# Performance work log

Hardware: AMD Instinct MI355X
Metric: run time of the kernel (lower is better)

The kernel has to match this reference:

```python
import jax, jax.numpy as jnp
import numpy as np

D_MODEL = 1024
NUM_HEADS = 16
D_K = D_MODEL // NUM_HEADS


def setup_inputs() -> dict:
    key = jax.random.key(0)
    ks = jax.random.split(key, 9)
    s = 1.0 / np.sqrt(D_MODEL)
    inp = {
        "x": jax.random.normal(ks[0], (2, 2048, D_MODEL), dtype=jnp.float32),
        "Wq": jax.random.uniform(ks[1], (D_MODEL, D_MODEL), jnp.float32, -s, s),
        "bq": jax.random.uniform(ks[2], (D_MODEL,), jnp.float32, -s, s),
        "Wk": jax.random.uniform(ks[3], (D_MODEL, D_MODEL), jnp.float32, -s, s),
        "bk": jax.random.uniform(ks[4], (D_MODEL,), jnp.float32, -s, s),
        "Wv": jax.random.uniform(ks[5], (D_MODEL, D_MODEL), jnp.float32, -s, s),
        "bv": jax.random.uniform(ks[6], (D_MODEL,), jnp.float32, -s, s),
        "Wo": jax.random.uniform(ks[7], (D_MODEL, D_MODEL), jnp.float32, -s, s),
        "bo": jax.random.uniform(ks[8], (D_MODEL,), jnp.float32, -s, s),
    }
    return inp


def reference(x, Wq, bq, Wk, bk, Wv, bv, Wo, bo):
    B, S, _ = x.shape
    # projections (torch Linear: y = x @ W.T + b)
    q = x @ Wq.T + bq
    k = x @ Wk.T + bk
    v = x @ Wv.T + bv
    # [B, H, S, Dk]
    q = q.reshape(B, S, NUM_HEADS, D_K).transpose(0, 2, 1, 3)
    k = k.reshape(B, S, NUM_HEADS, D_K).transpose(0, 2, 1, 3)
    v = v.reshape(B, S, NUM_HEADS, D_K).transpose(0, 2, 1, 3)
    scale = 1.0 / np.sqrt(D_K).astype(np.float32)
    energy = jnp.einsum("bhqd,bhkd->bhqk", q, k) * scale
    attn = jax.nn.softmax(energy, axis=-1)
    out = jnp.einsum("bhqk,bhkd->bhqd", attn, v)
    out = out.transpose(0, 2, 1, 3).reshape(B, S, D_MODEL)
    return out @ Wo.T + bo
```

## Files before the change

### kernel.cpp

```cpp
#include <hip/hip_runtime.h>
#include <hip/hip_bf16.h>
#include <cstdint>

typedef __bf16 bf16;
typedef __bf16 bf16x4 __attribute__((ext_vector_type(4)));
typedef __bf16 bf16x8 __attribute__((ext_vector_type(8)));
typedef float f32x4 __attribute__((ext_vector_type(4)));
typedef float f32x16 __attribute__((ext_vector_type(16)));
typedef unsigned int u32x4 __attribute__((ext_vector_type(4)));

#define DM   1024
#define SEQ  2048
#define NH   16
#define DKH  64

__device__ __forceinline__ bf16x8 ld8(const bf16* p) {
    return *reinterpret_cast<const bf16x8*>(p);
}

__device__ __forceinline__ void gld16(const void* g, void* lds) {
    __builtin_amdgcn_global_load_lds(
        (__attribute__((address_space(1))) void*)(uintptr_t)g,
        (__attribute__((address_space(3))) void*)(uint32_t)(uintptr_t)lds,
        16, 0, 0);
}

__device__ __forceinline__ f32x4 mfma16(bf16x8 a, bf16x8 b, f32x4 c) {
    return __builtin_amdgcn_mfma_f32_16x16x32_bf16(a, b, c, 0, 0, 0);
}
__device__ __forceinline__ f32x16 mfma32(bf16x8 a, bf16x8 b, f32x16 c) {
    return __builtin_amdgcn_mfma_f32_32x32x16_bf16(a, b, c, 0, 0, 0);
}

__device__ __forceinline__ unsigned pkbf(float lo, float hi) {
    unsigned r;
    asm("v_cvt_pk_bf16_f32 %0, %1, %2" : "=v"(r) : "v"(lo), "v"(hi));
    return r;
}
__device__ __forceinline__ void plswap(unsigned& a, unsigned& b) {
    asm volatile("v_permlane32_swap_b32 %0, %1" : "+v"(a), "+v"(b));
}

__global__ __launch_bounds__(256) void cvt_all(
    const float4* __restrict__ x,  const float4* __restrict__ wq,
    const float4* __restrict__ wk, const float4* __restrict__ wv,
    const float4* __restrict__ wo,
    ushort4* __restrict__ xb,  ushort4* __restrict__ wqb,
    ushort4* __restrict__ wkb, ushort4* __restrict__ wvb,
    ushort4* __restrict__ wob) {
    int i = blockIdx.x * 256 + threadIdx.x;
    const float4* src;
    ushort4* dst;
    int off;
    if (i < 1048576) {
        src = x; dst = xb; off = i;
    } else {
        int r = i - 1048576;
        int sel = r >> 18;
        off = r & 262143;
        src = sel == 0 ? wq : sel == 1 ? wk : sel == 2 ? wv : wo;
        dst = sel == 0 ? wqb : sel == 1 ? wkb : sel == 2 ? wvb : wob;
    }
    float4 f = src[off];
    ushort4 u;
    u.x = __builtin_bit_cast(unsigned short, (bf16)f.x);
    u.y = __builtin_bit_cast(unsigned short, (bf16)f.y);
    u.z = __builtin_bit_cast(unsigned short, (bf16)f.z);
    u.w = __builtin_bit_cast(unsigned short, (bf16)f.w);
    dst[off] = u;
}

template <int OUT_MODE>
__device__ __forceinline__ void gemm_body(const bf16* __restrict__ A,
                                          const bf16* __restrict__ W,
                                          const float* __restrict__ bias,
                                          void* __restrict__ outp,
                                          int m0, int n0, float scale,
                                          bf16* __restrict__ S) {
    constexpr int BK = 32;
    const int t    = threadIdx.x;
    const int lane = t & 63;
    const int r16  = lane & 15, grp = lane >> 4;
    const int wave = t >> 6;
    const int wr   = (wave >> 1) * 64;
    const int wc   = (wave & 1) * 64;

    f32x4 acc[4][4] = {};

    const int srow = t >> 2;
    const int scol = t & 3;

    auto STAGE = [&](int buf, int kt) {
#pragma unroll
        for (int i = 0; i < 2; ++i) {
            const int row = i * 64 + srow;
            const int cs = (scol ^ (row & 3)) * 8;
            gld16(A + (size_t)(m0 + row) * DM + kt * BK + cs,
                  &S[buf * 8192 + i * 2048 + t * 8]);
            gld16(W + (size_t)(n0 + row) * DM + kt * BK + cs,
                  &S[buf * 8192 + 4096 + i * 2048 + t * 8]);
        }
    };

    STAGE(0, 0);
    STAGE(1, 1);

#pragma unroll
    for (int kt = 0; kt < 32; ++kt) {
        if (kt == 31) { asm volatile("s_waitcnt vmcnt(0)" ::: "memory"); }
        else          { asm volatile("s_waitcnt vmcnt(4)" ::: "memory"); }
        __builtin_amdgcn_sched_barrier(0);
        __builtin_amdgcn_s_barrier();
        __builtin_amdgcn_sched_barrier(0);

        if (kt < 30) STAGE((kt + 2) % 3, kt + 2);

        const bf16* Ab = &S[(kt % 3) * 8192];
        const bf16* Bb = Ab + 4096;
        bf16x8 af[4], bfr[4];
#pragma unroll
        for (int m = 0; m < 4; ++m) {
            const int row = wr + m * 16 + r16;
            af[m] = ld8(&Ab[row * BK + ((grp ^ (row & 3)) * 8)]);
        }
#pragma unroll
        for (int n = 0; n < 4; ++n) {
            const int row = wc + n * 16 + r16;
            bfr[n] = ld8(&Bb[row * BK + ((grp ^ (row & 3)) * 8)]);
        }
        __builtin_amdgcn_s_setprio(1);
#pragma unroll
        for (int m = 0; m < 4; ++m)
#pragma unroll
            for (int n = 0; n < 4; ++n)
                acc[m][n] = mfma16(af[m], bfr[n], acc[m][n]);
        __builtin_amdgcn_s_setprio(0);
    }

    if constexpr (OUT_MODE == 2) {
        __syncthreads();
        bf16* Tw = &S[wave * 4096];
        const int b = m0 >> 11;
        const int tokbase = (m0 & 2047) + wr;
#pragma unroll
        for (int n = 0; n < 4; ++n) {
            const int dim = n * 16 + r16;
            const float bvv = bias[n0 - 2048 + wc + dim];
#pragma unroll
            for (int m = 0; m < 4; ++m) {
                bf16x4 w4 = {(bf16)(acc[m][n][0] + bvv), (bf16)(acc[m][n][1] + bvv),
                             (bf16)(acc[m][n][2] + bvv), (bf16)(acc[m][n][3] + bvv)};
                const int slot = (m * 2 + (grp >> 1)) ^ (dim & 7);
                *reinterpret_cast<bf16x4*>(&Tw[dim * 64 + slot * 8 + (grp & 1) * 4]) = w4;
            }
        }
        asm volatile("" ::: "memory");
#pragma unroll
        for (int r = 0; r < 8; ++r) {
            const int dim = (lane >> 3) + 8 * r;
            const int ts  = lane & 7;
            bf16x8 v = ld8(&Tw[dim * 64 + ((ts ^ (dim & 7)) * 8)]);
            const int col = n0 - 2048 + wc + dim;
            bf16* dst = (bf16*)outp +
                ((size_t)(b * NH + (col >> 6)) * DKH + (col & 63)) * SEQ +
                tokbase + ts * 8;
            *reinterpret_cast<bf16x8*>(dst) = v;
        }
    } else {
#pragma unroll
        for (int n = 0; n < 4; ++n) {
            const int col = (OUT_MODE == 0 ? (n0 & 1023) : n0) + wc + n * 16 + r16;
            const float bvv = bias[col];
#pragma unroll
            for (int m = 0; m < 4; ++m) {
                const int row = m0 + wr + m * 16 + grp * 4;
#pragma unroll
                for (int j = 0; j < 4; ++j) {
                    float v = (acc[m][n][j] + bvv) * scale;
                    if constexpr (OUT_MODE == 1)
                        ((float*)outp)[(size_t)(row + j) * DM + col] = v;
                    else
                        ((bf16*)outp)[(size_t)(row + j) * DM + col] = (bf16)v;
                }
            }
        }
    }
}

__global__ __launch_bounds__(256, 3) void gemm_qkv(
    const bf16* __restrict__ xb, const bf16* __restrict__ wqkv,
    const float* __restrict__ bq, const float* __restrict__ bk,
    const float* __restrict__ bv_,
    bf16* __restrict__ q, bf16* __restrict__ k, bf16* __restrict__ vt) {
    __shared__ __attribute__((aligned(16))) bf16 S[24576];
    int id = blockIdx.x;
    id = (id & 7) * 96 + (id >> 3);
    const int nt = id % 24, mt = id / 24;
    const int m0 = mt * 128, n0 = nt * 128;
    if (nt < 8) {
        gemm_body<0>(xb, wqkv, bq, q, m0, n0, 0.18033688f, S);
    } else if (nt < 16) {
        gemm_body<0>(xb, wqkv, bk, k, m0, n0, 1.0f, S);
    } else {
        gemm_body<2>(xb, wqkv, bv_, vt, m0, n0, 1.0f, S);
    }
}

__global__ __launch_bounds__(256, 3) void gemm_out(
    const bf16* __restrict__ ab, const bf16* __restrict__ wob,
    const float* __restrict__ bo, float* __restrict__ out) {
    __shared__ __attribute__((aligned(16))) bf16 S[24576];
    int id = blockIdx.x;
    id = (id & 7) * 32 + (id >> 3);
    const int m0 = (id >> 3) * 128, n0 = (id & 7) * 128;
    gemm_body<1>(ab, wob, bo, out, m0, n0, 1.0f, S);
}

__global__ __launch_bounds__(256) void attn(const bf16* __restrict__ Q,
                                            const bf16* __restrict__ K,
                                            const bf16* __restrict__ VT,
                                            bf16* __restrict__ O) {
    __shared__ __attribute__((aligned(16))) bf16 Ks[3][64 * 64];
    __shared__ __attribute__((aligned(16))) bf16 Vs[3][64 * 64];

    const int t = threadIdx.x, lane = t & 63, wave = t >> 6;
    const int l31 = lane & 31, hi = lane >> 5;

    int id = blockIdx.x;
    id = (id & 7) * 64 + (id >> 3);
    const int qt = id & 15, h = (id >> 4) & 15, b = id >> 8;

    const bf16* Qb = Q + ((size_t)b * SEQ + qt * 128) * DM + h * DKH;
    const bf16* Kb = K + (size_t)b * SEQ * DM + h * DKH;
    const bf16* Vb = VT + (size_t)((b * NH + h) * DKH) * SEQ;

    bf16x8 qf[4];
#pragma unroll
    for (int c = 0; c < 4; ++c)
        qf[c] = ld8(Qb + (size_t)(wave * 32 + l31) * DM + c * 16 + hi * 8);

    const bf16 one = (bf16)1.0f;
    const bf16x8 ones8 = {one, one, one, one, one, one, one, one};

    f32x16 o[2] = {};
    f32x16 ol = {};

    const int sr = t >> 3, scs = t & 7;

    auto STAGE = [&](int bsel, int tile) {
        const int kt = tile << 6;
#pragma unroll
        for (int i = 0; i < 2; ++i) {
            const int r = i * 32 + sr;
            const int cs = (scs ^ (r & 7)) * 8;
            gld16(Kb + (size_t)(kt + r) * DM + cs, &Ks[bsel][i * 2048 + t * 8]);
            gld16(Vb + (size_t)r * SEQ + kt + cs, &Vs[bsel][i * 2048 + t * 8]);
        }
    };

    auto TILE = [&](const bf16* KsB, const bf16* VsB) {
        u32x4 up[4];
#pragma unroll
        for (int sub = 0; sub < 2; ++sub) {
            const int krow = sub * 32 + l31;
            const int ksw  = krow & 7;
            f32x16 ss = {};
            __builtin_amdgcn_s_setprio(1);
#pragma unroll
            for (int c = 0; c < 4; ++c) {
                const bf16x8 kf = ld8(&KsB[krow * 64 + (((c * 2 + hi) ^ ksw) * 8)]);
                ss = mfma32(kf, qf[c], ss);
            }
            __builtin_amdgcn_s_setprio(0);
            float e[16];
#pragma unroll
            for (int r = 0; r < 16; ++r)
                e[r] = __builtin_amdgcn_exp2f(ss[r]);
            unsigned u0 = pkbf(e[0],  e[1]),  u1 = pkbf(e[2],  e[3]);
            unsigned u2 = pkbf(e[4],  e[5]),  u3 = pkbf(e[6],  e[7]);
            unsigned u4 = pkbf(e[8],  e[9]),  u5 = pkbf(e[10], e[11]);
            unsigned u6 = pkbf(e[12], e[13]), u7 = pkbf(e[14], e[15]);
            plswap(u0, u2); plswap(u1, u3);
            plswap(u4, u6); plswap(u5, u7);
            up[sub * 2]     = u32x4{u0, u1, u2, u3};
            up[sub * 2 + 1] = u32x4{u4, u5, u6, u7};
        }

        __builtin_amdgcn_s_setprio(1);
#pragma unroll
        for (int dt = 0; dt < 2; ++dt) {
            const int vrow = dt * 32 + l31;
            const int vsw  = vrow & 7;
#pragma unroll
            for (int kc = 0; kc < 4; ++kc) {
                const bf16x8 vf = ld8(&VsB[vrow * 64 + (((kc * 2 + hi) ^ vsw) * 8)]);
                o[dt] = mfma32(__builtin_bit_cast(bf16x8, up[kc]), vf, o[dt]);
            }
        }
#pragma unroll
        for (int kc = 0; kc < 4; ++kc)
            ol = mfma32(__builtin_bit_cast(bf16x8, up[kc]), ones8, ol);
        __builtin_amdgcn_s_setprio(0);
    };

#define GATE(N) do {                                              \
        asm volatile("s_waitcnt vmcnt(" #N ")" ::: "memory");     \
        __builtin_amdgcn_sched_barrier(0);                        \
        __builtin_amdgcn_s_barrier();                             \
        __builtin_amdgcn_sched_barrier(0);                        \
    } while (0)

    STAGE(0, 0);
    STAGE(1, 1);

    int nx = 2;
#pragma unroll 1
    for (int g = 0; g < 10; ++g) {
        GATE(4); STAGE(2, nx); ++nx; TILE(Ks[0], Vs[0]);
        GATE(4); STAGE(0, nx); ++nx; TILE(Ks[1], Vs[1]);
        GATE(4); STAGE(1, nx); ++nx; TILE(Ks[2], Vs[2]);
    }
    GATE(4); TILE(Ks[0], Vs[0]);
    GATE(0); TILE(Ks[1], Vs[1]);
#undef GATE

    float inv[16];
#pragma unroll
    for (int r = 0; r < 16; ++r)
        inv[r] = 1.0f / ol[r];
#pragma unroll
    for (int dt = 0; dt < 2; ++dt)
#pragma unroll
        for (int r = 0; r < 16; ++r) {
            const int ql = (r & 3) + 8 * (r >> 2) + 4 * hi;
            O[((size_t)b * SEQ + qt * 128 + wave * 32 + ql) * DM
              + h * DKH + dt * 32 + l31] = (bf16)(o[dt][r] * inv[r]);
        }
}

extern "C" void kernel_launch(void* const* d_in, const int* in_sizes, int n_in,
                              void* d_out, int out_size, void* d_ws, size_t ws_size,
                              hipStream_t stream) {
    const float* x  = (const float*)d_in[0];
    const float* Wq = (const float*)d_in[1];
    const float* bq = (const float*)d_in[2];
    const float* Wk = (const float*)d_in[3];
    const float* bk = (const float*)d_in[4];
    const float* Wv = (const float*)d_in[5];
    const float* bv = (const float*)d_in[6];
    const float* Wo = (const float*)d_in[7];
    const float* bo = (const float*)d_in[8];
    float* out = (float*)d_out;

    char* ws = (char*)d_ws;
    bf16* xb   = (bf16*)(ws + 0);
    bf16* wqkv = (bf16*)(ws + 8388608);
    bf16* wqb  = (bf16*)(ws + 8388608);
    bf16* wkb  = (bf16*)(ws + 10485760);
    bf16* wvb  = (bf16*)(ws + 12582912);
    bf16* wob  = (bf16*)(ws + 14680064);
    bf16* qb   = (bf16*)(ws + 16777216);
    bf16* kb   = (bf16*)(ws + 25165824);
    bf16* ab   = (bf16*)(ws + 33554432);
    bf16* vtb  = (bf16*)(ws + 41943040);

    cvt_all<<<8192, 256, 0, stream>>>(
        (const float4*)x, (const float4*)Wq, (const float4*)Wk,
        (const float4*)Wv, (const float4*)Wo,
        (ushort4*)xb, (ushort4*)wqb, (ushort4*)wkb, (ushort4*)wvb, (ushort4*)wob);

    gemm_qkv<<<768, 256, 0, stream>>>(xb, wqkv, bq, bk, bv, qb, kb, vtb);

    attn<<<dim3(512), 256, 0, stream>>>(qb, kb, vtb, ab);

    gemm_out<<<256, 256, 0, stream>>>(ab, wob, bo, out);
}
```

Before: 106.6 us.

## Split KV range across wave pairs in attention with register-blocked queries and LDS reduction

```diff
diff --git a/kernel.cpp b/kernel.cpp
--- a/kernel.cpp
+++ b/kernel.cpp
@@ -216,15 +216,16 @@
     gemm_body<1>(ab, wob, bo, out, m0, n0, 1.0f, S);
 }
 
-__global__ __launch_bounds__(256) void attn(const bf16* __restrict__ Q,
-                                            const bf16* __restrict__ K,
-                                            const bf16* __restrict__ VT,
-                                            bf16* __restrict__ O) {
-    __shared__ __attribute__((aligned(16))) bf16 Ks[3][64 * 64];
-    __shared__ __attribute__((aligned(16))) bf16 Vs[3][64 * 64];
+__global__ __launch_bounds__(256, 2) void attn(const bf16* __restrict__ Q,
+                                               const bf16* __restrict__ K,
+                                               const bf16* __restrict__ VT,
+                                               bf16* __restrict__ O) {
+    __shared__ __attribute__((aligned(16))) bf16 S[2][2][8192];
 
     const int t = threadIdx.x, lane = t & 63, wave = t >> 6;
     const int l31 = lane & 31, hi = lane >> 5;
+    const int kvh = wave >> 1;
+    const int qw  = wave & 1;
 
     int id = blockIdx.x;
     id = (id & 7) * 64 + (id >> 3);
@@ -234,56 +235,70 @@
     const bf16* Kb = K + (size_t)b * SEQ * DM + h * DKH;
     const bf16* Vb = VT + (size_t)((b * NH + h) * DKH) * SEQ;
 
-    bf16x8 qf[4];
-#pragma unroll
-    for (int c = 0; c < 4; ++c)
-        qf[c] = ld8(Qb + (size_t)(wave * 32 + l31) * DM + c * 16 + hi * 8);
+    bf16x8 qf[2][4];
+#pragma unroll
+    for (int u = 0; u < 2; ++u)
+#pragma unroll
+        for (int c = 0; c < 4; ++c)
+            qf[u][c] = ld8(Qb + (size_t)(qw * 64 + u * 32 + l31) * DM + c * 16 + hi * 8);
 
     const bf16 one = (bf16)1.0f;
     const bf16x8 ones8 = {one, one, one, one, one, one, one, one};
 
-    f32x16 o[2] = {};
-    f32x16 ol = {};
+    f32x16 o[2][2] = {};
+    f32x16 ol[2] = {};
 
     const int sr = t >> 3, scs = t & 7;
 
-    auto STAGE = [&](int bsel, int tile) {
-        const int kt = tile << 6;
-#pragma unroll
-        for (int i = 0; i < 2; ++i) {
-            const int r = i * 32 + sr;
-            const int cs = (scs ^ (r & 7)) * 8;
-            gld16(Kb + (size_t)(kt + r) * DM + cs, &Ks[bsel][i * 2048 + t * 8]);
-            gld16(Vb + (size_t)r * SEQ + kt + cs, &Vs[bsel][i * 2048 + t * 8]);
+    auto STAGE = [&](int buf, int step) {
+#pragma unroll
+        for (int hf = 0; hf < 2; ++hf) {
+            const int kt = hf * 1024 + step * 64;
+            bf16* Kd = &S[hf][buf][0];
+            bf16* Vd = &S[hf][buf][4096];
+#pragma unroll
+            for (int i = 0; i < 2; ++i) {
+                const int r = i * 32 + sr;
+                const int cs = (scs ^ (r & 7)) * 8;
+                gld16(Kb + (size_t)(kt + r) * DM + cs, Kd + i * 2048 + t * 8);
+                gld16(Vb + (size_t)r * SEQ + kt + cs, Vd + i * 2048 + t * 8);
+            }
         }
     };
 
     auto TILE = [&](const bf16* KsB, const bf16* VsB) {
-        u32x4 up[4];
+        u32x4 up[2][4];
 #pragma unroll
         for (int sub = 0; sub < 2; ++sub) {
             const int krow = sub * 32 + l31;
             const int ksw  = krow & 7;
-            f32x16 ss = {};
+            bf16x8 kf[4];
+#pragma unroll
+            for (int c = 0; c < 4; ++c)
+                kf[c] = ld8(&KsB[krow * 64 + (((c * 2 + hi) ^ ksw) * 8)]);
+            f32x16 ss0 = {}, ss1 = {};
             __builtin_amdgcn_s_setprio(1);
 #pragma unroll
-            for (int c = 0; c < 4; ++c) {
-                const bf16x8 kf = ld8(&KsB[krow * 64 + (((c * 2 + hi) ^ ksw) * 8)]);
-                ss = mfma32(kf, qf[c], ss);
-            }
+            for (int c = 0; c < 4; ++c) ss0 = mfma32(kf[c], qf[0][c], ss0);
+#pragma unroll
+            for (int c = 0; c < 4; ++c) ss1 = mfma32(kf[c], qf[1][c], ss1);
             __builtin_amdgcn_s_setprio(0);
-            float e[16];
-#pragma unroll
-            for (int r = 0; r < 16; ++r)
-                e[r] = __builtin_amdgcn_exp2f(ss[r]);
-            unsigned u0 = pkbf(e[0],  e[1]),  u1 = pkbf(e[2],  e[3]);
-            unsigned u2 = pkbf(e[4],  e[5]),  u3 = pkbf(e[6],  e[7]);
-            unsigned u4 = pkbf(e[8],  e[9]),  u5 = pkbf(e[10], e[11]);
-            unsigned u6 = pkbf(e[12], e[13]), u7 = pkbf(e[14], e[15]);
-            plswap(u0, u2); plswap(u1, u3);
-            plswap(u4, u6); plswap(u5, u7);
-            up[sub * 2]     = u32x4{u0, u1, u2, u3};
-            up[sub * 2 + 1] = u32x4{u4, u5, u6, u7};
+#pragma unroll
+            for (int u = 0; u < 2; ++u) {
+                const f32x16& ss = u ? ss1 : ss0;
+                float e[16];
+#pragma unroll
+                for (int r = 0; r < 16; ++r)
+                    e[r] = __builtin_amdgcn_exp2f(ss[r]);
+                unsigned u0 = pkbf(e[0],  e[1]),  u1 = pkbf(e[2],  e[3]);
+                unsigned u2 = pkbf(e[4],  e[5]),  u3 = pkbf(e[6],  e[7]);
+                unsigned u4 = pkbf(e[8],  e[9]),  u5 = pkbf(e[10], e[11]);
+                unsigned u6 = pkbf(e[12], e[13]), u7 = pkbf(e[14], e[15]);
+                plswap(u0, u2); plswap(u1, u3);
+                plswap(u4, u6); plswap(u5, u7);
+                up[u][sub * 2]     = u32x4{u0, u1, u2, u3};
+                up[u][sub * 2 + 1] = u32x4{u4, u5, u6, u7};
+            }
         }
 
         __builtin_amdgcn_s_setprio(1);
@@ -294,17 +309,23 @@
 #pragma unroll
             for (int kc = 0; kc < 4; ++kc) {
                 const bf16x8 vf = ld8(&VsB[vrow * 64 + (((kc * 2 + hi) ^ vsw) * 8)]);
-                o[dt] = mfma32(__builtin_bit_cast(bf16x8, up[kc]), vf, o[dt]);
-            }
-        }
-#pragma unroll
-        for (int kc = 0; kc < 4; ++kc)
-            ol = mfma32(__builtin_bit_cast(bf16x8, up[kc]), ones8, ol);
+                o[0][dt] = mfma32(__builtin_bit_cast(bf16x8, up[0][kc]), vf, o[0][dt]);
+                o[1][dt] = mfma32(__builtin_bit_cast(bf16x8, up[1][kc]), vf, o[1][dt]);
+            }
+        }
+#pragma unroll
+        for (int kc = 0; kc < 4; ++kc) {
+            ol[0] = mfma32(__builtin_bit_cast(bf16x8, up[0][kc]), ones8, ol[0]);
+            ol[1] = mfma32(__builtin_bit_cast(bf16x8, up[1][kc]), ones8, ol[1]);
+        }
         __builtin_amdgcn_s_setprio(0);
     };
 
 #define GATE(N) do {                                              \
         asm volatile("s_waitcnt vmcnt(" #N ")" ::: "memory");     \
+        __builtin_amdgcn_sched_barrier(0);                        \
+    } while (0)
+#define BAR() do {                                                \
         __builtin_amdgcn_sched_barrier(0);                        \
         __builtin_amdgcn_s_barrier();                             \
         __builtin_amdgcn_sched_barrier(0);                        \
@@ -313,29 +334,83 @@
     STAGE(0, 0);
     STAGE(1, 1);
 
-    int nx = 2;
+    GATE(8); TILE(&S[kvh][0][0], &S[kvh][0][4096]);
 #pragma unroll 1
-    for (int g = 0; g < 10; ++g) {
-        GATE(4); STAGE(2, nx); ++nx; TILE(Ks[0], Vs[0]);
-        GATE(4); STAGE(0, nx); ++nx; TILE(Ks[1], Vs[1]);
-        GATE(4); STAGE(1, nx); ++nx; TILE(Ks[2], Vs[2]);
-    }
-    GATE(4); TILE(Ks[0], Vs[0]);
-    GATE(0); TILE(Ks[1], Vs[1]);
+    for (int g = 0; g < 7; ++g) {
+        BAR(); STAGE(0, 2 * g + 2);
+        GATE(8); TILE(&S[kvh][1][0], &S[kvh][1][4096]);
+        BAR(); STAGE(1, 2 * g + 3);
+        GATE(8); TILE(&S[kvh][0][0], &S[kvh][0][4096]);
+    }
+    BAR();
+    GATE(0); TILE(&S[kvh][1][0], &S[kvh][1][4096]);
 #undef GATE
-
-    float inv[16];
-#pragma unroll
-    for (int r = 0; r < 16; ++r)
-        inv[r] = 1.0f / ol[r];
-#pragma unroll
-    for (int dt = 0; dt < 2; ++dt)
-#pragma unroll
-        for (int r = 0; r < 16; ++r) {
-            const int ql = (r & 3) + 8 * (r >> 2) + 4 * hi;
-            O[((size_t)b * SEQ + qt * 128 + wave * 32 + ql) * DM
-              + h * DKH + dt * 32 + l31] = (bf16)(o[dt][r] * inv[r]);
-        }
+#undef BAR
+
+    __syncthreads();
+    float* Xs = (float*)&S[0][0][0];
+    if (wave >= 2) {
+        float* base = Xs + (wave - 2) * 6144;
+#pragma unroll
+        for (int u = 0; u < 2; ++u)
+#pragma unroll
+            for (int dt = 0; dt < 2; ++dt)
+#pragma unroll
+                for (int g4 = 0; g4 < 4; ++g4) {
+                    f32x4 v = {o[u][dt][g4 * 4], o[u][dt][g4 * 4 + 1],
+                               o[u][dt][g4 * 4 + 2], o[u][dt][g4 * 4 + 3]};
+                    *reinterpret_cast<f32x4*>(
+                        base + ((u * 2 + dt) * 4 + g4) * 256 + lane * 4) = v;
+                }
+#pragma unroll
+        for (int u = 0; u < 2; ++u)
+#pragma unroll
+            for (int g4 = 0; g4 < 4; ++g4) {
+                f32x4 v = {ol[u][g4 * 4], ol[u][g4 * 4 + 1],
+                           ol[u][g4 * 4 + 2], ol[u][g4 * 4 + 3]};
+                *reinterpret_cast<f32x4*>(
+                    base + (16 + u * 4 + g4) * 256 + lane * 4) = v;
+            }
+    }
+    __syncthreads();
+    if (wave < 2) {
+        const float* base = Xs + wave * 6144;
+#pragma unroll
+        for (int u = 0; u < 2; ++u)
+#pragma unroll
+            for (int dt = 0; dt < 2; ++dt)
+#pragma unroll
+                for (int g4 = 0; g4 < 4; ++g4) {
+                    f32x4 v = *reinterpret_cast<const f32x4*>(
+                        base + ((u * 2 + dt) * 4 + g4) * 256 + lane * 4);
+#pragma unroll
+                    for (int j = 0; j < 4; ++j) o[u][dt][g4 * 4 + j] += v[j];
+                }
+#pragma unroll
+        for (int u = 0; u < 2; ++u)
+#pragma unroll
+            for (int g4 = 0; g4 < 4; ++g4) {
+                f32x4 v = *reinterpret_cast<const f32x4*>(
+                    base + (16 + u * 4 + g4) * 256 + lane * 4);
+#pragma unroll
+                for (int j = 0; j < 4; ++j) ol[u][g4 * 4 + j] += v[j];
+            }
+
+#pragma unroll
+        for (int u = 0; u < 2; ++u) {
+            float inv[16];
+#pragma unroll
+            for (int r = 0; r < 16; ++r) inv[r] = 1.0f / ol[u][r];
+#pragma unroll
+            for (int dt = 0; dt < 2; ++dt)
+#pragma unroll
+                for (int r = 0; r < 16; ++r) {
+                    const int ql = (r & 3) + 8 * (r >> 2) + 4 * hi;
+                    O[((size_t)b * SEQ + qt * 128 + qw * 64 + u * 32 + ql) * DM
+                      + h * DKH + dt * 32 + l31] = (bf16)(o[u][dt][r] * inv[r]);
+                }
+        }
+    }
 }
 
 extern "C" void kernel_launch(void* const* d_in, const int* in_sizes, int n_in,
```

New measurement: 105.4 us. About the same (-1.1%).
